# Kernel tuning notes

Hardware: AMD Instinct MI355X
Metric: run time of the kernel (lower is better)

Reference implementation:

```python
import jax, jax.numpy as jnp
import numpy as np

B = 32          # number of trees (batch)
N_LEAVES = 512  # complete binary tree -> 2*N_LEAVES-1 nodes per tree
IN_DIM = 1024
MEM = 1024


def setup_inputs() -> dict:
    key = jax.random.key(0)
    k1, k2, k3, k4 = jax.random.split(key, 4)
    s = 0.02
    inputs = jax.random.normal(k1, (B, N_LEAVES, IN_DIM), jnp.float32)
    w_fioux = jax.random.normal(k2, (4 * MEM, IN_DIM), jnp.float32) * s
    # rand_init: bias zero except first mem_dim entries set to 1 (forget-gate bias)
    b_fioux = jnp.zeros((4 * MEM,), jnp.float32).at[:MEM].set(1.0)
    w_iouh = jax.random.normal(k3, (3 * MEM, 2 * MEM), jnp.float32) * s
    w_fh = jax.random.normal(k4, (2 * MEM, 2 * MEM), jnp.float32) * s
    return {"inputs": inputs, "w_fioux": w_fioux, "b_fioux": b_fioux,
            "w_iouh": w_iouh, "w_fh": w_fh}


def _node_forward(x, child_c, child_h, w_fioux, b_fioux, w_iouh, w_fh):
    # x: [B, n, IN_DIM]; child_c/child_h: [B, n, 2*MEM] (left || right)
    fioux = x @ w_fioux.T + b_fioux                      # [B, n, 4M]
    fx, ix, ox, ux = jnp.split(fioux, 4, axis=-1)        # each [B, n, M]
    ih, oh, uh = jnp.split(child_h @ w_iouh.T, 3, axis=-1)
    i = jax.nn.sigmoid(ix + ih)
    o = jax.nn.sigmoid(ox + oh)
    u = jnp.tanh(ux + uh)
    # f gates: fx repeated for both children + fh(child_h)
    f = jax.nn.sigmoid(jnp.concatenate([fx, fx], axis=-1) + child_h @ w_fh.T)
    fc = f * child_c                                     # [B, n, 2M]
    c = i * u + fc[..., :MEM] + fc[..., MEM:]            # sum over the 2 children
    h = o * jnp.tanh(c)
    return c, h


def reference(inputs, w_fioux, b_fioux, w_iouh, w_fh):
    # Leaves: x = word input, child states are zeros
    z = jnp.zeros((B, N_LEAVES, 2 * MEM), inputs.dtype)
    c, h = _node_forward(inputs, z, z, w_fioux, b_fioux, w_iouh, w_fh)
    n = N_LEAVES
    # Internal nodes, level by level (log2(N_LEAVES) fixed iterations):
    # x = zeros (internal nodes have no token input), children are adjacent pairs.
    while n > 1:
        n //= 2
        child_c = c.reshape(B, n, 2 * MEM)   # [left_c || right_c]
        child_h = h.reshape(B, n, 2 * MEM)
        x = jnp.zeros((B, n, IN_DIM), inputs.dtype)
        c, h = _node_forward(x, child_c, child_h, w_fioux, b_fioux, w_iouh, w_fh)
    return h[:, 0, :]  # root hidden state, [B, MEM]
```

## Files before the change

kernel.cpp:

```cpp
#include <hip/hip_runtime.h>
#include <cstdint>
#include <cstddef>


typedef __attribute__((ext_vector_type(8))) short bf16x8;
typedef __attribute__((ext_vector_type(4))) float f32x4;

__device__ __forceinline__ float sig_(float x) { return 1.0f / (1.0f + __expf(-x)); }

__device__ __forceinline__ unsigned short f2bf_(float x) {
    union { float f; uint32_t u; } v; v.f = x;
    uint32_t r = v.u + 0x7fffu + ((v.u >> 16) & 1u);
    return (unsigned short)(r >> 16);
}
__device__ __forceinline__ float bf2f_(unsigned short u) {
    union { uint32_t u; float f; } v; v.u = ((uint32_t)u) << 16; return v.f;
}

#define GL16(g, l) __builtin_amdgcn_global_load_lds( \
    (const __attribute__((address_space(1))) void*)(g), \
    (__attribute__((address_space(3))) void*)(l), 16, 0, 0)

__global__ __launch_bounds__(256, 2)
void gemm_nodef(const unsigned short* __restrict__ A,
                const unsigned short* __restrict__ Wp,
                const float* __restrict__ b,
                const unsigned short* __restrict__ c_prev,
                unsigned short* __restrict__ c_out,
                unsigned short* __restrict__ h_out,
                int M)
{
    __shared__ unsigned short lA[3 * 4096];
    __shared__ unsigned short lB[3 * 5120];
    const int lda = 2048;

    const int orig = blockIdx.x + 32 * blockIdx.y;
    const int xcd  = orig & 7;
    const int pos  = orig >> 3;
    const int bx   = xcd * 4 + (pos & 3);
    const int by   = pos >> 2;

    if ((pos >> 5) & 1) asm volatile("s_sleep 10" ::: "memory");

    const int tid = threadIdx.x;
    const int ln  = tid & 63;
    const int wv  = tid >> 6;
    const int wrp = wv >> 1;
    const int wcp = wv & 1;
    const int row0 = by * 128;
    const int colb = bx * 160;
    const bool five = (wv < 2);

    const int rowS = tid >> 2;
    const int gS   = (tid & 3) ^ ((tid >> 3) & 3);
    const unsigned short* a0 = A + (size_t)(row0 + rowS) * lda + gS * 8;
    const unsigned short* a1 = a0 + (size_t)64 * lda;
    const unsigned short* w0 = Wp + (size_t)(colb + rowS) * lda + gS * 8;
    const unsigned short* w1 = w0 + (size_t)64 * lda;
    const unsigned short* w2 = w0 + (size_t)128 * lda;
    const int ld0 = tid * 8;

    int offA[4], offB[5];
    #pragma unroll
    for (int i = 0; i < 4; ++i) {
        const int r = wrp * 64 + i * 16 + (ln & 15);
        offA[i] = r * 32 + ((ln >> 4) ^ ((r >> 1) & 3)) * 8;
    }
    #pragma unroll
    for (int g = 0; g < 5; ++g) {
        const int r = wcp * 80 + g * 16 + (ln & 15);
        offB[g] = r * 32 + ((ln >> 4) ^ ((r >> 1) & 3)) * 8;
    }

    f32x4 acc[4][5] = {};
    const int P = 64;

#define ISSUE_N(sl, kh) do { \
    const size_t _ko = (size_t)(kh) * 32; \
    GL16(a0 + _ko, lA + (sl) * 4096 + ld0); \
    GL16(a1 + _ko, lA + (sl) * 4096 + 2048 + ld0); \
    GL16(w0 + _ko, lB + (sl) * 5120 + ld0); \
    GL16(w1 + _ko, lB + (sl) * 5120 + 2048 + ld0); \
    if (five) GL16(w2 + _ko, lB + (sl) * 5120 + 4096 + ld0); \
} while (0)

    ISSUE_N(0, 0); ISSUE_N(1, 1);
    if (five) asm volatile("s_waitcnt vmcnt(5)" ::: "memory");
    else      asm volatile("s_waitcnt vmcnt(4)" ::: "memory");
    asm volatile("s_barrier" ::: "memory");

    int rd = 0, is = 2;
    for (int p = 0; p < P; ++p) {
        const unsigned short* pa = lA + rd * 4096;
        const unsigned short* pb = lB + rd * 5120;
        bf16x8 bf[5], af[4];
        #pragma unroll
        for (int g = 0; g < 5; ++g) bf[g] = *(const bf16x8*)(pb + offB[g]);
        #pragma unroll
        for (int i = 0; i < 4; ++i) af[i] = *(const bf16x8*)(pa + offA[i]);
        if (p <= P - 3) ISSUE_N(is, p + 2);
        __builtin_amdgcn_s_setprio(1);
        #pragma unroll
        for (int m = 0; m < 4; ++m)
            #pragma unroll
            for (int g = 0; g < 5; ++g)
                acc[m][g] = __builtin_amdgcn_mfma_f32_16x16x32_bf16(af[m], bf[g], acc[m][g], 0, 0, 0);
        __builtin_amdgcn_s_setprio(0);
        if (p <= P - 3) {
            if (five) asm volatile("s_waitcnt vmcnt(5)" ::: "memory");
            else      asm volatile("s_waitcnt vmcnt(4)" ::: "memory");
        } else if (p == P - 2) {
            asm volatile("s_waitcnt vmcnt(0)" ::: "memory");
        }
        if (p < P - 1) asm volatile("s_barrier" ::: "memory");
        rd = (rd == 2) ? 0 : rd + 1;
        is = (is == 2) ? 0 : is + 1;
    }
#undef ISSUE_N

    const int jg = bx * 32 + wcp * 16 + (ln & 15);
    const float bi = b[1024 + jg];
    const float bo = b[2048 + jg];
    const float bu = b[3072 + jg];
    const float bff = b[jg];
    #pragma unroll
    for (int mi = 0; mi < 4; ++mi) {
        #pragma unroll
        for (int rg = 0; rg < 4; ++rg) {
            const int r = row0 + wrp * 64 + mi * 16 + (ln >> 4) * 4 + rg;
            const float cl = bf2f_(c_prev[(size_t)r * 2048 + jg]);
            const float cr = bf2f_(c_prev[(size_t)r * 2048 + 1024 + jg]);
            const float iv = sig_(acc[mi][0][rg] + bi);
            const float ov = sig_(acc[mi][1][rg] + bo);
            const float uv = tanhf(acc[mi][2][rg] + bu);
            const float flv = sig_(acc[mi][3][rg] + bff);
            const float frv = sig_(acc[mi][4][rg] + bff);
            const float c = iv * uv + flv * cl + frv * cr;
            const float h = ov * tanhf(c);
            c_out[(size_t)r * 1024 + jg] = f2bf_(c);
            h_out[(size_t)r * 1024 + jg] = f2bf_(h);
        }
    }
}

__global__ __launch_bounds__(256, 2)
void gemm_leaff(const unsigned short* __restrict__ A,
                const unsigned short* __restrict__ Wp,
                const float* __restrict__ b,
                unsigned short* __restrict__ c_out,
                unsigned short* __restrict__ h_out)
{
    __shared__ unsigned short lA[3 * 4096];
    __shared__ unsigned short lB[3 * 6144];
    const int lda = 1024;

    const int orig = blockIdx.x + 16 * blockIdx.y;
    const int xcd  = orig & 7;
    const int pos  = orig >> 3;
    const int bx   = xcd * 2 + (pos & 1);
    const int by   = pos >> 1;

    if ((pos >> 5) & 1) asm volatile("s_sleep 10" ::: "memory");

    const int tid = threadIdx.x;
    const int ln  = tid & 63;
    const int wv  = tid >> 6;
    const int wrp = wv >> 1;
    const int wcp = wv & 1;
    const int row0 = by * 128;
    const int colb = bx * 192;

    const int rowS = tid >> 2;
    const int gS   = (tid & 3) ^ ((tid >> 3) & 3);
    const unsigned short* a0 = A + (size_t)(row0 + rowS) * lda + gS * 8;
    const unsigned short* a1 = a0 + (size_t)64 * lda;
    const unsigned short* w0 = Wp + (size_t)(colb + rowS) * lda + gS * 8;
    const unsigned short* w1 = w0 + (size_t)64 * lda;
    const unsigned short* w2 = w0 + (size_t)128 * lda;
    const int ld0 = tid * 8;

    int offA[4], offB[6];
    #pragma unroll
    for (int i = 0; i < 4; ++i) {
        const int r = wrp * 64 + i * 16 + (ln & 15);
        offA[i] = r * 32 + ((ln >> 4) ^ ((r >> 1) & 3)) * 8;
    }
    #pragma unroll
    for (int grp = 0; grp < 2; ++grp)
        #pragma unroll
        for (int g = 0; g < 3; ++g) {
            const int r = wcp * 96 + grp * 48 + g * 16 + (ln & 15);
            offB[grp * 3 + g] = r * 32 + ((ln >> 4) ^ ((r >> 1) & 3)) * 8;
        }

    f32x4 acc[4][6] = {};
    const int P = 32;

#define ISSUE_L(sl, kh) do { \
    const size_t _ko = (size_t)(kh) * 32; \
    GL16(a0 + _ko, lA + (sl) * 4096 + ld0); \
    GL16(a1 + _ko, lA + (sl) * 4096 + 2048 + ld0); \
    GL16(w0 + _ko, lB + (sl) * 6144 + ld0); \
    GL16(w1 + _ko, lB + (sl) * 6144 + 2048 + ld0); \
    GL16(w2 + _ko, lB + (sl) * 6144 + 4096 + ld0); \
} while (0)

    ISSUE_L(0, 0); ISSUE_L(1, 1);
    asm volatile("s_waitcnt vmcnt(5)" ::: "memory");
    asm volatile("s_barrier" ::: "memory");

    int rd = 0, is = 2;
    for (int p = 0; p < P; ++p) {
        const unsigned short* pa = lA + rd * 4096;
        const unsigned short* pb = lB + rd * 6144;
        bf16x8 bf[6], af[4];
        #pragma unroll
        for (int g = 0; g < 6; ++g) bf[g] = *(const bf16x8*)(pb + offB[g]);
        #pragma unroll
        for (int i = 0; i < 4; ++i) af[i] = *(const bf16x8*)(pa + offA[i]);
        if (p <= P - 3) ISSUE_L(is, p + 2);
        __builtin_amdgcn_s_setprio(1);
        #pragma unroll
        for (int m = 0; m < 4; ++m)
            #pragma unroll
            for (int g = 0; g < 6; ++g)
                acc[m][g] = __builtin_amdgcn_mfma_f32_16x16x32_bf16(af[m], bf[g], acc[m][g], 0, 0, 0);
        __builtin_amdgcn_s_setprio(0);
        if (p <= P - 3)      asm volatile("s_waitcnt vmcnt(5)" ::: "memory");
        else if (p == P - 2) asm volatile("s_waitcnt vmcnt(0)" ::: "memory");
        if (p < P - 1) asm volatile("s_barrier" ::: "memory");
        rd = (rd == 2) ? 0 : rd + 1;
        is = (is == 2) ? 0 : is + 1;
    }
#undef ISSUE_L

    #pragma unroll
    for (int grp = 0; grp < 2; ++grp) {
        const int j = bx * 64 + wcp * 32 + grp * 16 + (ln & 15);
        const float bi = b[1024 + j];
        const float bo = b[2048 + j];
        const float bu = b[3072 + j];
        #pragma unroll
        for (int mi = 0; mi < 4; ++mi) {
            #pragma unroll
            for (int rg = 0; rg < 4; ++rg) {
                const int r = row0 + wrp * 64 + mi * 16 + (ln >> 4) * 4 + rg;
                const float cv = sig_(acc[mi][grp * 3 + 0][rg] + bi) * tanhf(acc[mi][grp * 3 + 2][rg] + bu);
                const float hv = sig_(acc[mi][grp * 3 + 1][rg] + bo) * tanhf(cv);
                c_out[(size_t)r * 1024 + j] = f2bf_(cv);
                h_out[(size_t)r * 1024 + j] = f2bf_(hv);
            }
        }
    }
}

__global__ __launch_bounds__(512, 2)
void gemm256(const unsigned short* __restrict__ A,
             const unsigned short* __restrict__ W,
             unsigned short* __restrict__ C, int M, int N, int lda, int Klen)
{
    __shared__ unsigned short lA[4 * 8192];
    __shared__ unsigned short lB[4 * 8192];

    const int gx = gridDim.x, gy = gridDim.y;
    int id = blockIdx.x + gx * (blockIdx.y + gy * blockIdx.z);
    {
        const int nwg = gx * gy * gridDim.z;
        const int q = nwg >> 3, r = nwg & 7, x = id & 7, i = id >> 3;
        id = (x < r ? x * (q + 1) : r * (q + 1) + (x - r) * q) + i;
    }
    const int bz  = id / (gx * gy);
    const int rem = id - bz * gx * gy;
    const int by  = rem / gx;
    const int bx  = rem - by * gx;

    const int tid = threadIdx.x;
    const int ln  = tid & 63;
    const int wv  = tid >> 6;
    const int wrp = wv >> 2;
    const int wcp = wv & 3;
    const int row0 = by * 256;
    const int colb = bx * 256;
    const int kbase = bz * Klen;
    C += (size_t)bz * M * N;

    const int rowS = tid >> 2;
    const int gS   = (tid & 3) ^ ((tid >> 3) & 3);
    const unsigned short* a0 = A + (size_t)min(row0 + rowS,       M - 1) * lda + kbase + gS * 8;
    const unsigned short* a1 = A + (size_t)min(row0 + rowS + 128, M - 1) * lda + kbase + gS * 8;
    const unsigned short* b0 = W + (size_t)(colb + rowS)       * lda + kbase + gS * 8;
    const unsigned short* b1 = W + (size_t)(colb + rowS + 128) * lda + kbase + gS * 8;
    const int ld0 = tid * 8;
    const int ld1 = tid * 8 + 4096;

    int offA[8], offB[4];
    #pragma unroll
    for (int i = 0; i < 8; ++i) {
        const int r = wrp * 128 + i * 16 + (ln & 15);
        offA[i] = r * 32 + ((ln >> 4) ^ ((r >> 1) & 3)) * 8;
    }
    #pragma unroll
    for (int i = 0; i < 4; ++i) {
        const int r = wcp * 64 + i * 16 + (ln & 15);
        offB[i] = r * 32 + ((ln >> 4) ^ ((r >> 1) & 3)) * 8;
    }

    f32x4 acc[8][4] = {};
    const int P = Klen >> 5;

#define ISSUE_KH(kh) do { \
    const int _sl = (kh) & 3; \
    const size_t _ko = (size_t)(kh) * 32; \
    GL16(a0 + _ko, lA + _sl * 8192 + ld0); \
    GL16(a1 + _ko, lA + _sl * 8192 + ld1); \
    GL16(b0 + _ko, lB + _sl * 8192 + ld0); \
    GL16(b1 + _ko, lB + _sl * 8192 + ld1); \
} while (0)

    ISSUE_KH(0); ISSUE_KH(1); ISSUE_KH(2);
    asm volatile("s_waitcnt vmcnt(8)" ::: "memory");
    asm volatile("s_barrier" ::: "memory");

    for (int p = 0; p < P; ++p) {
        const unsigned short* pa = lA + (p & 3) * 8192;
        const unsigned short* pb = lB + (p & 3) * 8192;
        bf16x8 bf[4], af[4], ag[4];
        #pragma unroll
        for (int i = 0; i < 4; ++i) bf[i] = *(const bf16x8*)(pb + offB[i]);
        #pragma unroll
        for (int i = 0; i < 4; ++i) af[i] = *(const bf16x8*)(pa + offA[i]);
        #pragma unroll
        for (int i = 0; i < 4; ++i) ag[i] = *(const bf16x8*)(pa + offA[4 + i]);
        if (p <= P - 4) ISSUE_KH(p + 3);
        __builtin_amdgcn_s_setprio(1);
        #pragma unroll
        for (int m = 0; m < 4; ++m)
            #pragma unroll
            for (int n = 0; n < 4; ++n)
                acc[m][n] = __builtin_amdgcn_mfma_f32_16x16x32_bf16(af[m], bf[n], acc[m][n], 0, 0, 0);
        #pragma unroll
        for (int m = 0; m < 4; ++m)
            #pragma unroll
            for (int n = 0; n < 4; ++n)
                acc[4 + m][n] = __builtin_amdgcn_mfma_f32_16x16x32_bf16(ag[m], bf[n], acc[4 + m][n], 0, 0, 0);
        __builtin_amdgcn_s_setprio(0);
        if (p <= P - 4)      asm volatile("s_waitcnt vmcnt(8)" ::: "memory");
        else if (p == P - 3) asm volatile("s_waitcnt vmcnt(4)" ::: "memory");
        else if (p == P - 2) asm volatile("s_waitcnt vmcnt(0)" ::: "memory");
        if (p < P - 1) asm volatile("s_barrier" ::: "memory");
    }
#undef ISSUE_KH

    #pragma unroll
    for (int mi = 0; mi < 8; ++mi) {
        #pragma unroll
        for (int ni = 0; ni < 4; ++ni) {
            const int col = colb + wcp * 64 + ni * 16 + (ln & 15);
            #pragma unroll
            for (int rg = 0; rg < 4; ++rg) {
                const int r = row0 + wrp * 128 + mi * 16 + (ln >> 4) * 4 + rg;
                if (r < M) C[(size_t)r * N + col] = f2bf_(acc[mi][ni][rg]);
            }
        }
    }
}

__global__ void f2bf_vec(const float* __restrict__ src, unsigned short* __restrict__ dst, int n4)
{
    const int i = blockIdx.x * blockDim.x + threadIdx.x;
    if (i >= n4) return;
    const float4 v = ((const float4*)src)[i];
    ushort4 o;
    o.x = f2bf_(v.x); o.y = f2bf_(v.y); o.z = f2bf_(v.z); o.w = f2bf_(v.w);
    ((ushort4*)dst)[i] = o;
}

__global__ void build_wfxp(const float* __restrict__ w_fioux,
                           unsigned short* __restrict__ dst, int total4)
{
    const int idx = blockIdx.x * blockDim.x + threadIdx.x;
    if (idx >= total4) return;
    const int rp = idx >> 8;
    const int c4 = (idx & 255) << 2;
    const int t  = rp / 48;
    const int q  = rp - t * 48;
    const int g  = q >> 4;
    const int jj = q & 15;
    const float* src = w_fioux + (size_t)((g + 1) * 1024 + t * 16 + jj) * 1024;
    const float4 v = *(const float4*)(src + c4);
    ushort4 o;
    o.x = f2bf_(v.x); o.y = f2bf_(v.y); o.z = f2bf_(v.z); o.w = f2bf_(v.w);
    *(ushort4*)(dst + (size_t)rp * 1024 + c4) = o;
}

__global__ void build_wcatp(const float* __restrict__ w_iouh, const float* __restrict__ w_fh,
                            unsigned short* __restrict__ dst, int total4)
{
    const int idx = blockIdx.x * blockDim.x + threadIdx.x;
    if (idx >= total4) return;
    const int rp = idx >> 9;
    const int c4 = (idx & 511) << 2;
    const int t  = rp / 80;
    const int q  = rp - t * 80;
    const int g  = q >> 4;
    const int jj = q & 15;
    const int srow = t * 16 + jj;
    const float* src = (g < 3) ? (w_iouh + (size_t)(g * 1024 + srow) * 2048)
                               : (w_fh   + (size_t)((g - 3) * 1024 + srow) * 2048);
    const float4 v = *(const float4*)(src + c4);
    ushort4 o;
    o.x = f2bf_(v.x); o.y = f2bf_(v.y); o.z = f2bf_(v.z); o.w = f2bf_(v.w);
    *(ushort4*)(dst + (size_t)rp * 2048 + c4) = o;
}

__device__ __forceinline__ void acc4_(float* v, ushort4 u) {
    v[0] += bf2f_(u.x); v[1] += bf2f_(u.y); v[2] += bf2f_(u.z); v[3] += bf2f_(u.w);
}

__global__ void node_gates(const unsigned short* __restrict__ g, int S, size_t sstride,
                           const float* __restrict__ b,
                           const unsigned short* __restrict__ c_prev,
                           unsigned short* __restrict__ c_out,
                           unsigned short* __restrict__ h_bf,
                           float* __restrict__ h_f32, int rows)
{
    const int idx = blockIdx.x * blockDim.x + threadIdx.x;
    if (idx >= rows * 256) return;
    const int r = idx >> 8, q = (idx & 255) << 2;
    const int t = q >> 4, jj = q & 15;
    float vi[4] = {}, vo[4] = {}, vu[4] = {}, vfl[4] = {}, vfr[4] = {};
    const unsigned short* gr = g + (size_t)r * 5120 + t * 80 + jj;
    for (int s = 0; s < S; ++s, gr += sstride) {
        acc4_(vi,  *(const ushort4*)(gr));
        acc4_(vo,  *(const ushort4*)(gr + 16));
        acc4_(vu,  *(const ushort4*)(gr + 32));
        acc4_(vfl, *(const ushort4*)(gr + 48));
        acc4_(vfr, *(const ushort4*)(gr + 64));
    }
    const float* bi = b + 1024 + q;
    const float* bo = b + 2048 + q;
    const float* bu = b + 3072 + q;
    const float* bff = b + q;
    const ushort4 clu = *(const ushort4*)(c_prev + (size_t)r * 2048 + q);
    const ushort4 cru = *(const ushort4*)(c_prev + (size_t)r * 2048 + 1024 + q);
    const float cl[4] = { bf2f_(clu.x), bf2f_(clu.y), bf2f_(clu.z), bf2f_(clu.w) };
    const float cr[4] = { bf2f_(cru.x), bf2f_(cru.y), bf2f_(cru.z), bf2f_(cru.w) };

    ushort4 co, ho;
    float cv[4], hv[4];
    #pragma unroll
    for (int e = 0; e < 4; ++e) {
        const float c = sig_(vi[e] + bi[e]) * tanhf(vu[e] + bu[e])
                      + sig_(vfl[e] + bff[e]) * cl[e]
                      + sig_(vfr[e] + bff[e]) * cr[e];
        cv[e] = c;
        hv[e] = sig_(vo[e] + bo[e]) * tanhf(c);
    }
    co.x = f2bf_(cv[0]); co.y = f2bf_(cv[1]); co.z = f2bf_(cv[2]); co.w = f2bf_(cv[3]);
    ho.x = f2bf_(hv[0]); ho.y = f2bf_(hv[1]); ho.z = f2bf_(hv[2]); ho.w = f2bf_(hv[3]);
    *(ushort4*)(c_out + (size_t)r * 1024 + q) = co;
    *(ushort4*)(h_bf + (size_t)r * 1024 + q) = ho;
    if (h_f32) {
        float4 hf; hf.x = hv[0]; hf.y = hv[1]; hf.z = hv[2]; hf.w = hv[3];
        *(float4*)(h_f32 + (size_t)r * 1024 + q) = hf;
    }
}

extern "C" void kernel_launch(void* const* d_in, const int* in_sizes, int n_in,
                              void* d_out, int out_size, void* d_ws, size_t ws_size,
                              hipStream_t stream)
{
    const float* inputs  = (const float*)d_in[0];
    const float* w_fioux = (const float*)d_in[1];
    const float* b_fioux = (const float*)d_in[2];
    const float* w_iouh  = (const float*)d_in[3];
    const float* w_fh    = (const float*)d_in[4];
    float* out = (float*)d_out;

    unsigned short* us    = (unsigned short*)d_ws;
    unsigned short* c_a   = us;
    unsigned short* c_b   = c_a + (size_t)16777216;
    unsigned short* h_a   = c_b + (size_t)8388608;
    unsigned short* h_b   = h_a + (size_t)16777216;
    unsigned short* wfxP  = h_b + (size_t)8388608;
    unsigned short* wcatP = wfxP + (size_t)3145728;
    unsigned short* gbuf  = wcatP + (size_t)10485760;
    unsigned short* x_bf  = gbuf;

    f2bf_vec<<<16384, 256, 0, stream>>>(inputs, x_bf, 4194304);
    build_wfxp<<<3072, 256, 0, stream>>>(w_fioux, wfxP, 786432);
    build_wcatp<<<10240, 256, 0, stream>>>(w_iouh, w_fh, wcatP, 5120 * 512);

    gemm_leaff<<<dim3(16, 128), 256, 0, stream>>>(x_bf, wfxP, b_fioux, c_a, h_a);

    unsigned short *hp = h_a, *cp = c_a, *hn = h_b, *cn = c_b;
    for (int n = 256; n >= 64; n >>= 1) {
        const int m = 32 * n;
        gemm_nodef<<<dim3(32, m / 128), 256, 0, stream>>>(hp, wcatP, b_fioux, cp, cn, hn, m);
        unsigned short* t;
        t = hp; hp = hn; hn = t;
        t = cp; cp = cn; cn = t;
    }

    for (int n = 32; n >= 1; n >>= 1) {
        const int m = 32 * n;
        const int S = (m >= 512) ? 4 : 8;
        const int Klen = 2048 / S;
        gemm256<<<dim3(20, (m + 255) / 256, S), 512, 0, stream>>>(
            hp, wcatP, gbuf, m, 5120, 2048, Klen);
        node_gates<<<m, 256, 0, stream>>>(
            gbuf, S, (size_t)m * 5120, b_fioux, cp, cn, hn,
            (n == 1) ? out : nullptr, m);
        unsigned short* t;
        t = hp; hp = hn; hn = t;
        t = cp; cp = cn; cn = t;
    }
    (void)in_sizes; (void)n_in; (void)out_size; (void)ws_size;
}
```

Measured before the change: 687.8 us.

## Enlarge fused node GEMM tile to 256x320 with 512 threads and deeper pipeline

```diff
diff --git a/kernel.cpp b/kernel.cpp
--- a/kernel.cpp
+++ b/kernel.cpp
@@ -21,49 +21,49 @@
     (const __attribute__((address_space(1))) void*)(g), \
     (__attribute__((address_space(3))) void*)(l), 16, 0, 0)
 
-__global__ __launch_bounds__(256, 2)
-void gemm_nodef(const unsigned short* __restrict__ A,
-                const unsigned short* __restrict__ Wp,
-                const float* __restrict__ b,
-                const unsigned short* __restrict__ c_prev,
-                unsigned short* __restrict__ c_out,
-                unsigned short* __restrict__ h_out,
-                int M)
-{
-    __shared__ unsigned short lA[3 * 4096];
-    __shared__ unsigned short lB[3 * 5120];
+__global__ __launch_bounds__(512, 2)
+void gemm320f(const unsigned short* __restrict__ A,
+              const unsigned short* __restrict__ Wp,
+              const float* __restrict__ b,
+              const unsigned short* __restrict__ c_prev,
+              unsigned short* __restrict__ c_out,
+              unsigned short* __restrict__ h_out,
+              int M)
+{
+    __shared__ unsigned short lA[4 * 8192];
+    __shared__ unsigned short lB[4 * 10240];
     const int lda = 2048;
 
-    const int orig = blockIdx.x + 32 * blockIdx.y;
+    const int orig = blockIdx.x + 16 * blockIdx.y;
     const int xcd  = orig & 7;
     const int pos  = orig >> 3;
-    const int bx   = xcd * 4 + (pos & 3);
-    const int by   = pos >> 2;
-
-    if ((pos >> 5) & 1) asm volatile("s_sleep 10" ::: "memory");
+    const int bx   = xcd * 2 + (pos & 1);
+    const int by   = pos >> 1;
 
     const int tid = threadIdx.x;
     const int ln  = tid & 63;
     const int wv  = tid >> 6;
-    const int wrp = wv >> 1;
-    const int wcp = wv & 1;
-    const int row0 = by * 128;
-    const int colb = bx * 160;
-    const bool five = (wv < 2);
+    const int wrp = wv >> 2;
+    const int wcp = wv & 3;
+    const int row0 = by * 256;
+    const int colb = bx * 320;
+    const bool five = (wv < 4);
 
     const int rowS = tid >> 2;
     const int gS   = (tid & 3) ^ ((tid >> 3) & 3);
-    const unsigned short* a0 = A + (size_t)(row0 + rowS) * lda + gS * 8;
-    const unsigned short* a1 = a0 + (size_t)64 * lda;
-    const unsigned short* w0 = Wp + (size_t)(colb + rowS) * lda + gS * 8;
-    const unsigned short* w1 = w0 + (size_t)64 * lda;
-    const unsigned short* w2 = w0 + (size_t)128 * lda;
+    const unsigned short* a0 = A + (size_t)min(row0 + rowS,       M - 1) * lda + gS * 8;
+    const unsigned short* a1 = A + (size_t)min(row0 + rowS + 128, M - 1) * lda + gS * 8;
+    const unsigned short* w0 = Wp + (size_t)(colb + rowS)       * lda + gS * 8;
+    const unsigned short* w1 = Wp + (size_t)(colb + rowS + 128) * lda + gS * 8;
+    const unsigned short* w2 = Wp + (size_t)(colb + 256 + ((tid & 255) >> 2)) * lda + gS * 8;
     const int ld0 = tid * 8;
-
-    int offA[4], offB[5];
-    #pragma unroll
-    for (int i = 0; i < 4; ++i) {
-        const int r = wrp * 64 + i * 16 + (ln & 15);
+    const int ld1 = tid * 8 + 4096;
+    const int ld2 = (tid & 255) * 8 + 8192;
+
+    int offA[8], offB[5];
+    #pragma unroll
+    for (int i = 0; i < 8; ++i) {
+        const int r = wrp * 128 + i * 16 + (ln & 15);
         offA[i] = r * 32 + ((ln >> 4) ^ ((r >> 1) & 3)) * 8;
     }
     #pragma unroll
@@ -72,73 +72,93 @@
         offB[g] = r * 32 + ((ln >> 4) ^ ((r >> 1) & 3)) * 8;
     }
 
-    f32x4 acc[4][5] = {};
+    f32x4 acc[8][5] = {};
     const int P = 64;
 
-#define ISSUE_N(sl, kh) do { \
+#define ISSUE_F(kh) do { \
+    const int _sl = (kh) & 3; \
     const size_t _ko = (size_t)(kh) * 32; \
-    GL16(a0 + _ko, lA + (sl) * 4096 + ld0); \
-    GL16(a1 + _ko, lA + (sl) * 4096 + 2048 + ld0); \
-    GL16(w0 + _ko, lB + (sl) * 5120 + ld0); \
-    GL16(w1 + _ko, lB + (sl) * 5120 + 2048 + ld0); \
-    if (five) GL16(w2 + _ko, lB + (sl) * 5120 + 4096 + ld0); \
+    GL16(a0 + _ko, lA + _sl * 8192 + ld0); \
+    GL16(a1 + _ko, lA + _sl * 8192 + ld1); \
+    GL16(w0 + _ko, lB + _sl * 10240 + ld0); \
+    GL16(w1 + _ko, lB + _sl * 10240 + ld1); \
+    if (five) GL16(w2 + _ko, lB + _sl * 10240 + ld2); \
 } while (0)
 
-    ISSUE_N(0, 0); ISSUE_N(1, 1);
+    ISSUE_F(0); ISSUE_F(1); ISSUE_F(2);
     if (five) asm volatile("s_waitcnt vmcnt(5)" ::: "memory");
     else      asm volatile("s_waitcnt vmcnt(4)" ::: "memory");
     asm volatile("s_barrier" ::: "memory");
 
-    int rd = 0, is = 2;
+    bf16x8 bcur[5], bnxt[5];
+    {
+        const unsigned short* pb0 = lB;
+        #pragma unroll
+        for (int g = 0; g < 5; ++g) bcur[g] = *(const bf16x8*)(pb0 + offB[g]);
+    }
+
     for (int p = 0; p < P; ++p) {
-        const unsigned short* pa = lA + rd * 4096;
-        const unsigned short* pb = lB + rd * 5120;
-        bf16x8 bf[5], af[4];
-        #pragma unroll
-        for (int g = 0; g < 5; ++g) bf[g] = *(const bf16x8*)(pb + offB[g]);
+        const unsigned short* pa  = lA + (p & 3) * 8192;
+        const unsigned short* pbn = lB + ((p + 1) & 3) * 10240;
+        bf16x8 af[4], ag[4];
         #pragma unroll
         for (int i = 0; i < 4; ++i) af[i] = *(const bf16x8*)(pa + offA[i]);
-        if (p <= P - 3) ISSUE_N(is, p + 2);
+        #pragma unroll
+        for (int i = 0; i < 4; ++i) ag[i] = *(const bf16x8*)(pa + offA[4 + i]);
+        if (p <= P - 4) ISSUE_F(p + 3);
+        if (p < P - 1) {
+            #pragma unroll
+            for (int g = 0; g < 5; ++g) bnxt[g] = *(const bf16x8*)(pbn + offB[g]);
+        }
         __builtin_amdgcn_s_setprio(1);
         #pragma unroll
         for (int m = 0; m < 4; ++m)
             #pragma unroll
             for (int g = 0; g < 5; ++g)
-                acc[m][g] = __builtin_amdgcn_mfma_f32_16x16x32_bf16(af[m], bf[g], acc[m][g], 0, 0, 0);
+                acc[m][g] = __builtin_amdgcn_mfma_f32_16x16x32_bf16(af[m], bcur[g], acc[m][g], 0, 0, 0);
+        #pragma unroll
+        for (int m = 0; m < 4; ++m)
+            #pragma unroll
+            for (int g = 0; g < 5; ++g)
+                acc[4 + m][g] = __builtin_amdgcn_mfma_f32_16x16x32_bf16(ag[m], bcur[g], acc[4 + m][g], 0, 0, 0);
         __builtin_amdgcn_s_setprio(0);
-        if (p <= P - 3) {
+        if (p <= P - 4) {
             if (five) asm volatile("s_waitcnt vmcnt(5)" ::: "memory");
             else      asm volatile("s_waitcnt vmcnt(4)" ::: "memory");
-        } else if (p == P - 2) {
+        } else if (p == P - 3) {
             asm volatile("s_waitcnt vmcnt(0)" ::: "memory");
         }
-        if (p < P - 1) asm volatile("s_barrier" ::: "memory");
-        rd = (rd == 2) ? 0 : rd + 1;
-        is = (is == 2) ? 0 : is + 1;
-    }
-#undef ISSUE_N
-
-    const int jg = bx * 32 + wcp * 16 + (ln & 15);
+        if (p < P - 1) {
+            asm volatile("s_barrier" ::: "memory");
+            #pragma unroll
+            for (int g = 0; g < 5; ++g) bcur[g] = bnxt[g];
+        }
+    }
+#undef ISSUE_F
+
+    const int jg = bx * 64 + wcp * 16 + (ln & 15);
     const float bi = b[1024 + jg];
     const float bo = b[2048 + jg];
     const float bu = b[3072 + jg];
     const float bff = b[jg];
     #pragma unroll
-    for (int mi = 0; mi < 4; ++mi) {
+    for (int mi = 0; mi < 8; ++mi) {
         #pragma unroll
         for (int rg = 0; rg < 4; ++rg) {
-            const int r = row0 + wrp * 64 + mi * 16 + (ln >> 4) * 4 + rg;
-            const float cl = bf2f_(c_prev[(size_t)r * 2048 + jg]);
-            const float cr = bf2f_(c_prev[(size_t)r * 2048 + 1024 + jg]);
-            const float iv = sig_(acc[mi][0][rg] + bi);
-            const float ov = sig_(acc[mi][1][rg] + bo);
-            const float uv = tanhf(acc[mi][2][rg] + bu);
-            const float flv = sig_(acc[mi][3][rg] + bff);
-            const float frv = sig_(acc[mi][4][rg] + bff);
-            const float c = iv * uv + flv * cl + frv * cr;
-            const float h = ov * tanhf(c);
-            c_out[(size_t)r * 1024 + jg] = f2bf_(c);
-            h_out[(size_t)r * 1024 + jg] = f2bf_(h);
+            const int r = row0 + wrp * 128 + mi * 16 + (ln >> 4) * 4 + rg;
+            if (r < M) {
+                const float cl = bf2f_(c_prev[(size_t)r * 2048 + jg]);
+                const float cr = bf2f_(c_prev[(size_t)r * 2048 + 1024 + jg]);
+                const float iv = sig_(acc[mi][0][rg] + bi);
+                const float ov = sig_(acc[mi][1][rg] + bo);
+                const float uv = tanhf(acc[mi][2][rg] + bu);
+                const float flv = sig_(acc[mi][3][rg] + bff);
+                const float frv = sig_(acc[mi][4][rg] + bff);
+                const float c = iv * uv + flv * cl + frv * cr;
+                const float h = ov * tanhf(c);
+                c_out[(size_t)r * 1024 + jg] = f2bf_(c);
+                h_out[(size_t)r * 1024 + jg] = f2bf_(h);
+            }
         }
     }
 }
@@ -496,7 +516,7 @@
     unsigned short *hp = h_a, *cp = c_a, *hn = h_b, *cn = c_b;
     for (int n = 256; n >= 64; n >>= 1) {
         const int m = 32 * n;
-        gemm_nodef<<<dim3(32, m / 128), 256, 0, stream>>>(hp, wcatP, b_fioux, cp, cn, hn, m);
+        gemm320f<<<dim3(16, m / 256), 512, 0, stream>>>(hp, wcatP, b_fioux, cp, cn, hn, m);
         unsigned short* t;
         t = hp; hp = hn; hn = t;
         t = cp; cp = cn; cn = t;
```

Result: slower. 775.1 us (+12.7%).
